# Performance work log

Measured on AMD Instinct MI355X. Metric: run time of the kernel, lower is better.

The kernel has to match this reference:

```python
import jax, jax.numpy as jnp
import numpy as np

NEG_FILL = -1000.0

def setup_inputs() -> dict:
    key = jax.random.key(0)
    k1, k2, k3, k4 = jax.random.split(key, 4)
    B, N, D = 16, 2048, 64
    q = jax.random.normal(k1, (B, N, D), dtype=jnp.float32)
    k = jax.random.normal(k2, (B, N, D), dtype=jnp.float32)
    v = jax.random.normal(k3, (B, N, D), dtype=jnp.float32)
    mask = jax.random.randint(k4, (B, N, N), 0, 2) == 1
    return {"q": q, "k": k, "v": v, "mask": mask}

def reference(q, k, v, mask):
    # Faithful to the torch module: scale by sqrt(seq_len) = len(q[0])**0.5,
    # masked positions set to -1000.0, softmax over dim=1 (NOT the last dim).
    seq_len = q.shape[1]
    scores = jnp.einsum('bnd,bmd->bnm', q, k) / jnp.sqrt(jnp.float32(seq_len))
    scores = jnp.where(mask, NEG_FILL, scores)
    attn = jax.nn.softmax(scores, axis=1)  # dim=1 as in nn.Softmax(dim=1)
    out = jnp.einsum('bnm,bmd->bnd', attn, v)
    return out
```

## Files before the change

### kernel.cpp

```cpp
#include <hip/hip_runtime.h>
#include <hip/hip_bf16.h>


#define B_ 16
#define N_ 2048
#define D_ 64
#define SCALE 0.022097086912079608f
#define NCH 8

typedef __attribute__((ext_vector_type(8))) short bf16x8;
typedef __attribute__((ext_vector_type(4))) float f32x4;

static __device__ __forceinline__ short f2bf(float x) {
  unsigned u = __float_as_uint(x);
  return (short)((u + 0x7FFF + ((u >> 16) & 1)) >> 16);
}

static __device__ __forceinline__ bf16x8 load8(const short* p) {
  return *reinterpret_cast<const bf16x8*>(p);
}

static __device__ __forceinline__ bf16x8 load8f(const float* p) {
  const f32x4 a = *reinterpret_cast<const f32x4*>(p);
  const f32x4 b = *reinterpret_cast<const f32x4*>(p + 4);
  bf16x8 r;
  r[0] = f2bf(a[0]); r[1] = f2bf(a[1]); r[2] = f2bf(a[2]); r[3] = f2bf(a[3]);
  r[4] = f2bf(b[0]); r[5] = f2bf(b[1]); r[6] = f2bf(b[2]); r[7] = f2bf(b[3]);
  return r;
}

__global__ __launch_bounds__(256) void cvt_bf16(const float* __restrict__ q,
                                                const float* __restrict__ k,
                                                short* __restrict__ qb,
                                                short* __restrict__ kb) {
  const size_t i = ((size_t)blockIdx.x * 256 + threadIdx.x) * 8;
  const float* src = blockIdx.y ? k : q;
  short* dst = blockIdx.y ? kb : qb;
  *reinterpret_cast<bf16x8*>(dst + i) = load8f(src + i);
}

__global__ __launch_bounds__(256) void score_kernel(
    const short* __restrict__ qb, const short* __restrict__ kb,
    const int* __restrict__ mask, short* __restrict__ pstore,
    float* __restrict__ csp) {
  const int b = blockIdx.x;
  const int wave = threadIdx.x >> 6;
  const int lane = threadIdx.x & 63;
  const int l15 = lane & 15;
  const int lhi = lane >> 4;
  const int m0 = blockIdx.y * 128 + wave * 32;
  const int mi = m0 >> 5;
  const int nbase = blockIdx.z * (N_ / NCH);

  const short* qbb = qb + (size_t)b * N_ * D_;
  const short* kbb = kb + (size_t)b * N_ * D_;
  const int* maskb = mask + (size_t)b * N_ * N_;

  bf16x8 kf[2][2];
#pragma unroll
  for (int cg = 0; cg < 2; ++cg) {
    kf[cg][0] = load8(kbb + (m0 + cg * 16 + l15) * D_ + lhi * 8);
    kf[cg][1] = load8(kbb + (m0 + cg * 16 + l15) * D_ + 32 + lhi * 8);
  }

  __shared__ __align__(16) short pbuf[4][16][40];

  float cs0 = 0.f, cs1 = 0.f;

  for (int n0 = nbase; n0 < nbase + N_ / NCH; n0 += 16) {
    int mk[2][4];
#pragma unroll
    for (int cg = 0; cg < 2; ++cg)
#pragma unroll
      for (int r = 0; r < 4; ++r)
        mk[cg][r] =
            maskb[(size_t)(n0 + lhi * 4 + r) * N_ + m0 + cg * 16 + l15];
    const bf16x8 qf0 = load8(qbb + (n0 + l15) * D_ + lhi * 8);
    const bf16x8 qf1 = load8(qbb + (n0 + l15) * D_ + 32 + lhi * 8);
#pragma unroll
    for (int cg = 0; cg < 2; ++cg) {
      f32x4 acc = {0.f, 0.f, 0.f, 0.f};
      acc = __builtin_amdgcn_mfma_f32_16x16x32_bf16(qf0, kf[cg][0], acc, 0, 0, 0);
      acc = __builtin_amdgcn_mfma_f32_16x16x32_bf16(qf1, kf[cg][1], acc, 0, 0, 0);
      float cp = 0.f;
#pragma unroll
      for (int r = 0; r < 4; ++r) {
        const float p = mk[cg][r] ? 0.f : __expf(acc[r] * SCALE);
        cp += p;
        pbuf[wave][lhi * 4 + r][cg * 16 + l15] = f2bf(p);
      }
      if (cg == 0) cs0 += cp; else cs1 += cp;
    }
    const bf16x8 pa =
        *reinterpret_cast<const bf16x8*>(&pbuf[wave][l15][lhi * 8]);
    const int n16 = n0 >> 4;
    *reinterpret_cast<bf16x8*>(
        pstore + (((size_t)b * 128 + n16) * 64 + mi) * 512 + lane * 8) = pa;
  }

  cs0 += __shfl_xor(cs0, 16, 64);
  cs0 += __shfl_xor(cs0, 32, 64);
  cs1 += __shfl_xor(cs1, 16, 64);
  cs1 += __shfl_xor(cs1, 32, 64);
  float* cspz = csp + ((size_t)b * NCH + blockIdx.z) * N_;
  if (lane < 16) {
    cspz[m0 + l15] = cs0;
    cspz[m0 + 16 + l15] = cs1;
  }
}

__global__ __launch_bounds__(256) void vprep_kernel(
    const float* __restrict__ v, const float* __restrict__ csp,
    short* __restrict__ vt) {
  const int b = blockIdx.x;
  const int m0 = blockIdx.y * 64;
  const int tid = threadIdx.x;
  __shared__ float csl[4][64];
  __shared__ float cst[64];
  __shared__ float lds[64][65];

  {
    const int col = m0 + (tid & 63);
    const int q4 = tid >> 6;
    float s = 0.f;
#pragma unroll
    for (int j = 0; j < 2; ++j)
      s += csp[((size_t)b * NCH + q4 * 2 + j) * N_ + col];
    csl[q4][tid & 63] = s;
  }
  __syncthreads();
  if (tid < 64) cst[tid] = csl[0][tid] + csl[1][tid] + csl[2][tid] + csl[3][tid];
  __syncthreads();

  const float* vb = v + (size_t)b * N_ * D_;
#pragma unroll
  for (int pass = 0; pass < 4; ++pass) {
    const int mloc = pass * 16 + (tid >> 4);
    const int d4 = (tid & 15) * 4;
    const f32x4 x = *reinterpret_cast<const f32x4*>(vb + (m0 + mloc) * D_ + d4);
    const float ic = 1.0f / cst[mloc];
    lds[mloc][d4 + 0] = x[0] * ic;
    lds[mloc][d4 + 1] = x[1] * ic;
    lds[mloc][d4 + 2] = x[2] * ic;
    lds[mloc][d4 + 3] = x[3] * ic;
  }
  __syncthreads();
  const int d = tid >> 2;
  const int seg = tid & 3;
  bf16x8 o0, o1;
#pragma unroll
  for (int i = 0; i < 8; ++i) o0[i] = f2bf(lds[seg * 16 + i][d]);
#pragma unroll
  for (int i = 0; i < 8; ++i) o1[i] = f2bf(lds[seg * 16 + 8 + i][d]);
  short* dst = vt + (size_t)b * D_ * N_ + (size_t)d * N_ + m0 + seg * 16;
  *reinterpret_cast<bf16x8*>(dst) = o0;
  *reinterpret_cast<bf16x8*>(dst + 8) = o1;
}

__global__ __launch_bounds__(256) void pv_kernel(const short* __restrict__ pstore,
                                                 const short* __restrict__ vt,
                                                 float* __restrict__ out) {
  const int b = blockIdx.x;
  const int wave = threadIdx.x >> 6;
  const int lane = threadIdx.x & 63;
  const int l15 = lane & 15;
  const int lhi = lane >> 4;
  const int n0 = blockIdx.y * 64 + wave * 16;
  const int n16 = blockIdx.y * 4 + wave;

  const short* psb =
      pstore + (((size_t)b * 128 + n16) * 64) * 512 + (size_t)lane * 8;
  const short* vtb = vt + (size_t)b * D_ * N_;

  f32x4 oacc[4];
#pragma unroll
  for (int d = 0; d < 4; ++d) oacc[d] = (f32x4){0.f, 0.f, 0.f, 0.f};

#pragma unroll 4
  for (int mi = 0; mi < 64; ++mi) {
    const bf16x8 pa = load8(psb + (size_t)mi * 512);
    const int m0 = mi * 32;
#pragma unroll
    for (int dsub = 0; dsub < 4; ++dsub) {
      const bf16x8 vf =
          load8(vtb + (size_t)(dsub * 16 + l15) * N_ + m0 + lhi * 8);
      oacc[dsub] =
          __builtin_amdgcn_mfma_f32_16x16x32_bf16(pa, vf, oacc[dsub], 0, 0, 0);
    }
  }

  float* dst = out + (size_t)b * N_ * D_;
#pragma unroll
  for (int dsub = 0; dsub < 4; ++dsub)
#pragma unroll
    for (int r = 0; r < 4; ++r)
      dst[(size_t)(n0 + lhi * 4 + r) * D_ + dsub * 16 + l15] = oacc[dsub][r];
}

__global__ __launch_bounds__(256) void colsum_fb(
    const float* __restrict__ q, const float* __restrict__ k,
    const int* __restrict__ mask, float* __restrict__ colsum) {
  const int b = blockIdx.x;
  const int wave = threadIdx.x >> 6;
  const int lane = threadIdx.x & 63;
  const int l15 = lane & 15;
  const int lhi = lane >> 4;
  const int m0 = blockIdx.y * 64 + wave * 16;
  const float* qbp = q + (size_t)b * N_ * D_;
  const float* kbp = k + (size_t)b * N_ * D_;
  const int* maskb = mask + (size_t)b * N_ * N_;
  const bf16x8 kf0 = load8f(kbp + (m0 + l15) * D_ + lhi * 8);
  const bf16x8 kf1 = load8f(kbp + (m0 + l15) * D_ + 32 + lhi * 8);
  float partial = 0.f;
  for (int n0 = 0; n0 < N_; n0 += 16) {
    bf16x8 qf0 = load8f(qbp + (n0 + l15) * D_ + lhi * 8);
    bf16x8 qf1 = load8f(qbp + (n0 + l15) * D_ + 32 + lhi * 8);
    f32x4 acc = {0.f, 0.f, 0.f, 0.f};
    acc = __builtin_amdgcn_mfma_f32_16x16x32_bf16(qf0, kf0, acc, 0, 0, 0);
    acc = __builtin_amdgcn_mfma_f32_16x16x32_bf16(qf1, kf1, acc, 0, 0, 0);
#pragma unroll
    for (int r = 0; r < 4; ++r) {
      const int n = n0 + lhi * 4 + r;
      partial +=
          maskb[(size_t)n * N_ + m0 + l15] ? 0.f : __expf(acc[r] * SCALE);
    }
  }
  partial += __shfl_xor(partial, 16, 64);
  partial += __shfl_xor(partial, 32, 64);
  if (lane < 16) colsum[(size_t)b * N_ + m0 + l15] = partial;
}

__global__ __launch_bounds__(256) void attn_out_fb(
    const float* __restrict__ q, const float* __restrict__ k,
    const float* __restrict__ v, const int* __restrict__ mask,
    const float* __restrict__ colsum, float* __restrict__ out) {
  const int b = blockIdx.x;
  const int wave = threadIdx.x >> 6;
  const int lane = threadIdx.x & 63;
  const int l15 = lane & 15;
  const int lhi = lane >> 4;
  const int n0 = blockIdx.y * 64 + wave * 16;
  const float* qbp = q + (size_t)b * N_ * D_;
  const float* kbp = k + (size_t)b * N_ * D_;
  const float* vbp = v + (size_t)b * N_ * D_;
  const int* maskb = mask + (size_t)b * N_ * N_;
  const float* csb = colsum + (size_t)b * N_;
  const bf16x8 qf0 = load8f(qbp + (n0 + l15) * D_ + lhi * 8);
  const bf16x8 qf1 = load8f(qbp + (n0 + l15) * D_ + 32 + lhi * 8);
  __shared__ __align__(16) short pbuf[4][16][32];
  f32x4 oacc[4];
#pragma unroll
  for (int d = 0; d < 4; ++d) oacc[d] = (f32x4){0.f, 0.f, 0.f, 0.f};
  for (int m0 = 0; m0 < N_; m0 += 32) {
#pragma unroll
    for (int cg = 0; cg < 2; ++cg) {
      const int mc = m0 + cg * 16;
      bf16x8 kf0 = load8f(kbp + (mc + l15) * D_ + lhi * 8);
      bf16x8 kf1 = load8f(kbp + (mc + l15) * D_ + 32 + lhi * 8);
      f32x4 acc = {0.f, 0.f, 0.f, 0.f};
      acc = __builtin_amdgcn_mfma_f32_16x16x32_bf16(qf0, kf0, acc, 0, 0, 0);
      acc = __builtin_amdgcn_mfma_f32_16x16x32_bf16(qf1, kf1, acc, 0, 0, 0);
      const float ic = 1.0f / csb[mc + l15];
#pragma unroll
      for (int r = 0; r < 4; ++r) {
        const int n = n0 + lhi * 4 + r;
        const float p = maskb[(size_t)n * N_ + mc + l15]
                            ? 0.f
                            : __expf(acc[r] * SCALE) * ic;
        pbuf[wave][lhi * 4 + r][cg * 16 + l15] = f2bf(p);
      }
    }
    __syncthreads();
    const bf16x8 pa =
        *reinterpret_cast<const bf16x8*>(&pbuf[wave][l15][lhi * 8]);
#pragma unroll
    for (int dsub = 0; dsub < 4; ++dsub) {
      bf16x8 vf;
#pragma unroll
      for (int j = 0; j < 8; ++j)
        vf[j] = f2bf(vbp[(m0 + lhi * 8 + j) * D_ + dsub * 16 + l15]);
      oacc[dsub] =
          __builtin_amdgcn_mfma_f32_16x16x32_bf16(pa, vf, oacc[dsub], 0, 0, 0);
    }
    __syncthreads();
  }
#pragma unroll
  for (int dsub = 0; dsub < 4; ++dsub)
#pragma unroll
    for (int r = 0; r < 4; ++r)
      out[(size_t)b * N_ * D_ + (size_t)(n0 + lhi * 4 + r) * D_ + dsub * 16 +
          l15] = oacc[dsub][r];
}

extern "C" void kernel_launch(void* const* d_in, const int* in_sizes, int n_in,
                              void* d_out, int out_size, void* d_ws,
                              size_t ws_size, hipStream_t stream) {
  const float* q = (const float*)d_in[0];
  const float* k = (const float*)d_in[1];
  const float* v = (const float*)d_in[2];
  const int* mask = (const int*)d_in[3];
  float* out = (float*)d_out;

  const size_t MB = 1024 * 1024;
  const size_t qb_off = 0;
  const size_t kb_off = qb_off + 4 * MB;
  const size_t vt_off = kb_off + 4 * MB;
  const size_t cs_off = vt_off + 4 * MB;
  const size_t ps_off = cs_off + 1 * MB;
  const size_t need = ps_off + 128 * MB;

  if (ws_size >= need) {
    short* qbf = (short*)((char*)d_ws + qb_off);
    short* kbf = (short*)((char*)d_ws + kb_off);
    short* vt = (short*)((char*)d_ws + vt_off);
    float* csp = (float*)((char*)d_ws + cs_off);
    short* pstore = (short*)((char*)d_ws + ps_off);

    cvt_bf16<<<dim3((B_ * N_ * D_) / (256 * 8), 2), 256, 0, stream>>>(
        q, k, qbf, kbf);
    score_kernel<<<dim3(B_, N_ / 128, NCH), 256, 0, stream>>>(qbf, kbf, mask,
                                                              pstore, csp);
    vprep_kernel<<<dim3(B_, N_ / 64), 256, 0, stream>>>(v, csp, vt);
    pv_kernel<<<dim3(B_, N_ / 64), 256, 0, stream>>>(pstore, vt, out);
  } else {
    float* colsum = (float*)d_ws;
    colsum_fb<<<dim3(B_, N_ / 64), 256, 0, stream>>>(q, k, mask, colsum);
    attn_out_fb<<<dim3(B_, N_ / 64), 256, 0, stream>>>(q, k, v, mask, colsum,
                                                       out);
  }
}
```

Before: 466.6 us.

## Recompute scores in PV pass from bit-packed mask instead of storing bf16 probabilities

The score pass now writes only a packed mask byte per lane (8 bits per 16x32 tile fragment) instead of a 128 MB bf16 probability tensor. The output kernel recomputes QK^T with MFMA, applies exp and the packed mask, and routes the probabilities through LDS into the PV MFMA. This trades a large global write and read of P for recomputing the scores and exponentials a second time. The mask is still read once at full int32 size.

Result: slower. 498.4 us (+6.8%).

```diff
diff --git a/kernel.cpp b/kernel.cpp
--- a/kernel.cpp
+++ b/kernel.cpp
@@ -10,6 +10,7 @@
 
 typedef __attribute__((ext_vector_type(8))) short bf16x8;
 typedef __attribute__((ext_vector_type(4))) float f32x4;
+typedef unsigned char u8;
 
 static __device__ __forceinline__ short f2bf(float x) {
   unsigned u = __float_as_uint(x);
@@ -39,9 +40,9 @@
   *reinterpret_cast<bf16x8*>(dst + i) = load8f(src + i);
 }
 
-__global__ __launch_bounds__(256) void score_kernel(
+__global__ __launch_bounds__(256) void cspack_kernel(
     const short* __restrict__ qb, const short* __restrict__ kb,
-    const int* __restrict__ mask, short* __restrict__ pstore,
+    const int* __restrict__ mask, u8* __restrict__ pk,
     float* __restrict__ csp) {
   const int b = blockIdx.x;
   const int wave = threadIdx.x >> 6;
@@ -63,8 +64,6 @@
     kf[cg][1] = load8(kbb + (m0 + cg * 16 + l15) * D_ + 32 + lhi * 8);
   }
 
-  __shared__ __align__(16) short pbuf[4][16][40];
-
   float cs0 = 0.f, cs1 = 0.f;
 
   for (int n0 = nbase; n0 < nbase + N_ / NCH; n0 += 16) {
@@ -77,6 +76,7 @@
             maskb[(size_t)(n0 + lhi * 4 + r) * N_ + m0 + cg * 16 + l15];
     const bf16x8 qf0 = load8(qbb + (n0 + l15) * D_ + lhi * 8);
     const bf16x8 qf1 = load8(qbb + (n0 + l15) * D_ + 32 + lhi * 8);
+    unsigned pbyte = 0;
 #pragma unroll
     for (int cg = 0; cg < 2; ++cg) {
       f32x4 acc = {0.f, 0.f, 0.f, 0.f};
@@ -87,15 +87,12 @@
       for (int r = 0; r < 4; ++r) {
         const float p = mk[cg][r] ? 0.f : __expf(acc[r] * SCALE);
         cp += p;
-        pbuf[wave][lhi * 4 + r][cg * 16 + l15] = f2bf(p);
+        pbyte |= (mk[cg][r] ? 1u : 0u) << (cg * 4 + r);
       }
       if (cg == 0) cs0 += cp; else cs1 += cp;
     }
-    const bf16x8 pa =
-        *reinterpret_cast<const bf16x8*>(&pbuf[wave][l15][lhi * 8]);
     const int n16 = n0 >> 4;
-    *reinterpret_cast<bf16x8*>(
-        pstore + (((size_t)b * 128 + n16) * 64 + mi) * 512 + lane * 8) = pa;
+    pk[(((size_t)b * 128 + n16) * 64 + mi) * 64 + lane] = (u8)pbyte;
   }
 
   cs0 += __shfl_xor(cs0, 16, 64);
@@ -157,29 +154,60 @@
   *reinterpret_cast<bf16x8*>(dst + 8) = o1;
 }
 
-__global__ __launch_bounds__(256) void pv_kernel(const short* __restrict__ pstore,
-                                                 const short* __restrict__ vt,
-                                                 float* __restrict__ out) {
+__global__ __launch_bounds__(256) void out2_kernel(
+    const short* __restrict__ qb, const short* __restrict__ kb,
+    const u8* __restrict__ pk, const short* __restrict__ vt,
+    float* __restrict__ out) {
   const int b = blockIdx.x;
   const int wave = threadIdx.x >> 6;
   const int lane = threadIdx.x & 63;
   const int l15 = lane & 15;
   const int lhi = lane >> 4;
-  const int n0 = blockIdx.y * 64 + wave * 16;
   const int n16 = blockIdx.y * 4 + wave;
-
-  const short* psb =
-      pstore + (((size_t)b * 128 + n16) * 64) * 512 + (size_t)lane * 8;
+  const int n0 = n16 * 16;
+
+  const short* qbb = qb + (size_t)b * N_ * D_;
+  const short* kbb = kb + (size_t)b * N_ * D_;
   const short* vtb = vt + (size_t)b * D_ * N_;
 
+  const bf16x8 qf0 = load8(qbb + (n0 + l15) * D_ + lhi * 8);
+  const bf16x8 qf1 = load8(qbb + (n0 + l15) * D_ + 32 + lhi * 8);
+
+  __shared__ __align__(16) u8 pks[4][4096];
+  __shared__ __align__(16) short pbuf[4][16][40];
+  {
+    const f32x4* src = reinterpret_cast<const f32x4*>(
+        pk + ((size_t)b * 128 + n16) * 4096);
+    f32x4* dst = reinterpret_cast<f32x4*>(pks[wave]);
+#pragma unroll
+    for (int j = 0; j < 4; ++j) dst[j * 64 + lane] = src[j * 64 + lane];
+  }
+
   f32x4 oacc[4];
 #pragma unroll
   for (int d = 0; d < 4; ++d) oacc[d] = (f32x4){0.f, 0.f, 0.f, 0.f};
 
-#pragma unroll 4
+#pragma unroll 2
   for (int mi = 0; mi < 64; ++mi) {
-    const bf16x8 pa = load8(psb + (size_t)mi * 512);
     const int m0 = mi * 32;
+    const unsigned pbyte = pks[wave][mi * 64 + lane];
+#pragma unroll
+    for (int cg = 0; cg < 2; ++cg) {
+      const bf16x8 kf0 = load8(kbb + (m0 + cg * 16 + l15) * D_ + lhi * 8);
+      const bf16x8 kf1 = load8(kbb + (m0 + cg * 16 + l15) * D_ + 32 + lhi * 8);
+      f32x4 acc = {0.f, 0.f, 0.f, 0.f};
+      acc = __builtin_amdgcn_mfma_f32_16x16x32_bf16(qf0, kf0, acc, 0, 0, 0);
+      acc = __builtin_amdgcn_mfma_f32_16x16x32_bf16(qf1, kf1, acc, 0, 0, 0);
+#pragma unroll
+      for (int r = 0; r < 4; ++r) {
+        const float p = ((pbyte >> (cg * 4 + r)) & 1u)
+                            ? 0.f
+                            : __expf(acc[r] * SCALE);
+        pbuf[wave][lhi * 4 + r][cg * 16 + l15] = f2bf(p);
+      }
+    }
+    const bf16x8 pa =
+        *reinterpret_cast<const bf16x8*>(&pbuf[wave][l15][lhi * 8]);
 #pragma unroll
     for (int dsub = 0; dsub < 4; ++dsub) {
       const bf16x8 vf =
@@ -306,22 +334,22 @@
   const size_t kb_off = qb_off + 4 * MB;
   const size_t vt_off = kb_off + 4 * MB;
   const size_t cs_off = vt_off + 4 * MB;
-  const size_t ps_off = cs_off + 1 * MB;
-  const size_t need = ps_off + 128 * MB;
+  const size_t pk_off = cs_off + 1 * MB;
+  const size_t need = pk_off + 8 * MB;
 
   if (ws_size >= need) {
     short* qbf = (short*)((char*)d_ws + qb_off);
     short* kbf = (short*)((char*)d_ws + kb_off);
     short* vt = (short*)((char*)d_ws + vt_off);
     float* csp = (float*)((char*)d_ws + cs_off);
-    short* pstore = (short*)((char*)d_ws + ps_off);
+    u8* pk = (u8*)((char*)d_ws + pk_off);
 
     cvt_bf16<<<dim3((B_ * N_ * D_) / (256 * 8), 2), 256, 0, stream>>>(
         q, k, qbf, kbf);
-    score_kernel<<<dim3(B_, N_ / 128, NCH), 256, 0, stream>>>(qbf, kbf, mask,
-                                                              pstore, csp);
+    cspack_kernel<<<dim3(B_, N_ / 128, NCH), 256, 0, stream>>>(qbf, kbf, mask,
+                                                               pk, csp);
     vprep_kernel<<<dim3(B_, N_ / 64), 256, 0, stream>>>(v, csp, vt);
-    pv_kernel<<<dim3(B_, N_ / 64), 256, 0, stream>>>(pstore, vt, out);
+    out2_kernel<<<dim3(B_, N_ / 64), 256, 0, stream>>>(qbf, kbf, pk, vt, out);
   } else {
     float* colsum = (float*)d_ws;
     colsum_fb<<<dim3(B_, N_ / 64), 256, 0, stream>>>(q, k, mask, colsum);
```
